# Kernel tuning notes

Measured on AMD Instinct MI355X. Metric: run time of the kernel, lower is better.

## Reference

```python
import jax, jax.numpy as jnp
import numpy as np

B, C_IN, C_OUT, K, H, W = 8, 512, 512, 3, 32, 32
EPS = 1e-8


def _fir_filter():
    f1 = jnp.array([1.0, 3.0, 3.0, 1.0], dtype=jnp.float32)
    f = jnp.outer(f1, f1)
    f = f / f.sum()
    return f * 4.0  # gain = 2**2, filter.ndim/2 == 1


def setup_inputs() -> dict:
    key = jax.random.key(0)
    k1, k2, k3 = jax.random.split(key, 3)
    x = jax.random.normal(k1, (B, C_IN, H, W), dtype=jnp.float32)
    styles = jax.random.normal(k2, (B, C_IN), dtype=jnp.float32)
    w = jax.random.normal(k3, (C_OUT, C_IN, K, K), dtype=jnp.float32)  # lr_multiplier=1
    return {"x": x, "styles": styles, "w": w}


def reference(x, styles, w):
    batch = x.shape[0]
    gain = 1.0 / np.sqrt(C_OUT * C_IN * K * K)
    # modulate: [B, O, I, kh, kw]
    wm = (w[None] * gain) * (styles[:, None, :, None, None] + 1.0)
    # demodulate
    dcoefs = jax.lax.rsqrt(jnp.sum(wm * wm, axis=(2, 3, 4)) + EPS)  # [B, O]
    wm = wm * dcoefs[:, :, None, None, None]
    # fused modconv: batch folded into channels/groups
    x1 = x.reshape(1, batch * C_IN, H, W)
    # torch conv_transpose2d(stride=2, padding=0, groups=B) == dilated conv with
    # spatially flipped kernel, lhs_dilation=2, padding=K-1 on each side.
    w_eq = jnp.flip(wm, axis=(-2, -1)).reshape(batch * C_OUT, C_IN, K, K)
    y = jax.lax.conv_general_dilated(
        x1, w_eq,
        window_strides=(1, 1),
        padding=[(K - 1, K - 1), (K - 1, K - 1)],
        lhs_dilation=(2, 2),
        feature_group_count=batch,
        dimension_numbers=("NCHW", "OIHW", "NCHW"),
    )  # [1, B*O, 2H+1, 2W+1]
    # Upfirdn2d: up=1, down=1, pad=[1,1,1,1], depthwise 4x4 FIR (cross-correlation;
    # filter is symmetric so no flip needed)
    C = batch * C_OUT
    f = jnp.broadcast_to(_fir_filter()[None, None], (C, 1, 4, 4))
    y = jax.lax.conv_general_dilated(
        y, f,
        window_strides=(1, 1),
        padding=[(1, 1), (1, 1)],
        feature_group_count=C,
        dimension_numbers=("NCHW", "OIHW", "NCHW"),
    )  # [1, B*O, 2H, 2W]
    return y.reshape(batch, C_OUT, 2 * H, 2 * W)
```

## Files before the change

### kernel.cpp

```cpp
#include <hip/hip_runtime.h>
#include <stdint.h>


#define DI __device__ __forceinline__

typedef __bf16 bf16x8 __attribute__((ext_vector_type(8)));
typedef float f32x4 __attribute__((ext_vector_type(4)));

DI float bf2f(ushort u) { union { uint32_t i; float f; } v; v.i = ((uint32_t)u) << 16; return v.f; }
DI ushort f2bf(float f) {
  union { float f; uint32_t i; } v; v.f = f;
  uint32_t x = v.i;
  return (ushort)((x + 0x7FFFu + ((x >> 16) & 1u)) >> 16);
}

#define GAIN (1.0f / 1536.0f)

__global__ __launch_bounds__(256) void k_prep(const float* __restrict__ w,
                                              const float* __restrict__ styles,
                                              const float* __restrict__ x,
                                              ushort* __restrict__ Wm,
                                              ushort* __restrict__ xt) {
  __shared__ union {
    struct { float ss[4096]; float dc[8]; float wred[4][8]; } wp;
    float tl[32][257];
  } sm;
  const int t = threadIdx.x;
  if (blockIdx.x < 512) {
    const int o = blockIdx.x;
#pragma unroll
    for (int j = 0; j < 4; j++) {
      const int idx = (t + j * 256) * 4;
      *(float4*)&sm.wp.ss[idx] = *(const float4*)&styles[idx];
    }
    float wreg[18];
    const float* wp_ = w + o * 4608 + t * 18;
#pragma unroll
    for (int k = 0; k < 9; k++) {
      float2 v2 = *(const float2*)(wp_ + 2 * k);
      wreg[2 * k] = v2.x;
      wreg[2 * k + 1] = v2.y;
    }
    float q0 = 0.f, q1 = 0.f;
#pragma unroll
    for (int k = 0; k < 9; k++) {
      q0 += wreg[k] * wreg[k];
      q1 += wreg[9 + k] * wreg[9 + k];
    }
    __syncthreads();
    float pb[8];
#pragma unroll
    for (int b = 0; b < 8; b++) {
      float s0 = sm.wp.ss[b * 512 + 2 * t] + 1.0f;
      float s1 = sm.wp.ss[b * 512 + 2 * t + 1] + 1.0f;
      pb[b] = s0 * s0 * q0 + s1 * s1 * q1;
    }
#pragma unroll
    for (int b = 0; b < 8; b++)
#pragma unroll
      for (int off = 32; off > 0; off >>= 1) pb[b] += __shfl_down(pb[b], off, 64);
    const int wid = t >> 6, lane = t & 63;
    if (lane == 0) {
#pragma unroll
      for (int b = 0; b < 8; b++) sm.wp.wred[wid][b] = pb[b];
    }
    __syncthreads();
    if (t < 8)
      sm.wp.dc[t] = rsqrtf((sm.wp.wred[0][t] + sm.wp.wred[1][t] + sm.wp.wred[2][t] + sm.wp.wred[3][t]) *
                               (GAIN * GAIN) + 1e-8f);
    __syncthreads();
#pragma unroll
    for (int b = 0; b < 8; b++) {
      const float d = sm.wp.dc[b];
      const float s0 = GAIN * (sm.wp.ss[b * 512 + 2 * t] + 1.0f) * d;
      const float s1 = GAIN * (sm.wp.ss[b * 512 + 2 * t + 1] + 1.0f) * d;
      ushort* base = Wm + ((size_t)(b * 9) * 512 + o) * 512 + 2 * t;
#pragma unroll
      for (int tap = 0; tap < 9; tap++) {
        ushort2 val = make_ushort2(f2bf(wreg[tap] * s0), f2bf(wreg[9 + tap] * s1));
        *(ushort2*)(base + (size_t)tap * 262144) = val;
      }
    }
  } else {
    const int idx = blockIdx.x - 512;
    const int hw0 = (idx & 3) * 256, i0 = ((idx >> 2) & 15) * 32, b = idx >> 6;
    const float* xb = x + b * (512 * 1024);
#pragma unroll
    for (int p = 0; p < 8; p++) {
      const int r = p * 4 + (t >> 6);
      const int c4 = (t & 63) * 4;
      float4 v = *(const float4*)&xb[(i0 + r) * 1024 + hw0 + c4];
      sm.tl[r][c4] = v.x; sm.tl[r][c4 + 1] = v.y; sm.tl[r][c4 + 2] = v.z; sm.tl[r][c4 + 3] = v.w;
    }
    __syncthreads();
    ushort* xtb = xt + b * (1024 * 512);
#pragma unroll
    for (int p = 0; p < 8; p++) {
      const int hw = p * 32 + (t >> 3);
      const int i4 = (t & 7) * 4;
      ushort4 v = make_ushort4(f2bf(sm.tl[i4][hw]), f2bf(sm.tl[i4 + 1][hw]),
                               f2bf(sm.tl[i4 + 2][hw]), f2bf(sm.tl[i4 + 3][hw]));
      *(ushort4*)&xtb[(hw0 + hw) * 512 + i0 + i4] = v;
    }
  }
}

__global__ __launch_bounds__(512, 4) void k_gemm(const ushort* __restrict__ A,
                                                 const ushort* __restrict__ Bt,
                                                 ushort* __restrict__ C) {
  __shared__ __attribute__((aligned(128))) char smem[49152];
  const int id = blockIdx.x;
  const int batch = id & 7;
  const int rem = id >> 3;
  const int mt = rem >> 2, nt = rem & 3;
  const int m0 = mt * 128, n0 = nt * 256;
  const ushort* Ag = A + (size_t)batch * (4608 * 512);
  const ushort* Bg = Bt + (size_t)batch * (1024 * 512);
  ushort* Cg = C + (size_t)batch * (4608 * 1024);

  const int tid = threadIdx.x;
  const int w = tid >> 6, lane = tid & 63;
  const int wm = w >> 2, wn = w & 3;
  const int lq = lane >> 4, l15 = lane & 15;

  const int srow = lane >> 2;
  const int sslot = (lane & 3) ^ ((lane >> 3) & 3);
  const char* gsrc[3];
  int ldst[3];
#pragma unroll
  for (int q = 0; q < 3; ++q) {
    const int idx = 3 * w + q;
    const bool isA = idx < 8;
    const int ch = isA ? idx : idx - 8;
    const int grow = (isA ? m0 : n0) + ch * 16 + srow;
    gsrc[q] = (const char*)(isA ? Ag : Bg) + (size_t)grow * 1024 + sslot * 16;
    ldst[q] = (isA ? 0 : 8192) + ch * 1024;
  }

#define GLL(srcp, dstp)                                                                     \
  __builtin_amdgcn_global_load_lds((const __attribute__((address_space(1))) void*)(srcp),   \
                                   (__attribute__((address_space(3))) void*)(dstp), 16, 0, 0)
#define ISSUE(buf, kt)                                              \
  do {                                                              \
    _Pragma("unroll")                                               \
    for (int q = 0; q < 3; ++q)                                     \
      GLL(gsrc[q] + (kt) * 64, smem + (buf) * 24576 + ldst[q]);     \
  } while (0)
#define CF asm volatile("" ::: "memory")
#define BAR()                          \
  do {                                 \
    CF;                                \
    __builtin_amdgcn_s_barrier();      \
    CF;                                \
  } while (0)

  const int so = (lq ^ ((l15 >> 1) & 3)) * 16;
  const char* Ard = smem + (wm * 64 + l15) * 64 + so;
  const char* Brd = smem + 8192 + (wn * 64 + l15) * 64 + so;

  f32x4 acc[4][4];
  const f32x4 z4 = {0.f, 0.f, 0.f, 0.f};
#pragma unroll
  for (int i = 0; i < 4; ++i)
#pragma unroll
    for (int n = 0; n < 4; ++n) acc[i][n] = z4;

  ISSUE(0, 0);
  asm volatile("s_waitcnt vmcnt(0)" ::: "memory");
  BAR();

#pragma unroll 2
  for (int t = 0; t < 16; ++t) {
    const int buf = t & 1;
    if (t < 15) ISSUE(buf ^ 1, t + 1);
    bf16x8 a[4], b[4];
#pragma unroll
    for (int i = 0; i < 4; ++i) a[i] = *(const bf16x8*)(Ard + buf * 24576 + i * 1024);
#pragma unroll
    for (int n = 0; n < 4; ++n) b[n] = *(const bf16x8*)(Brd + buf * 24576 + n * 1024);
    __builtin_amdgcn_s_setprio(1);
#pragma unroll
    for (int n = 0; n < 4; ++n)
#pragma unroll
      for (int i = 0; i < 4; ++i)
        acc[i][n] = __builtin_amdgcn_mfma_f32_16x16x32_bf16(a[i], b[n], acc[i][n], 0, 0, 0);
    __builtin_amdgcn_s_setprio(0);
    if (t < 15) asm volatile("s_waitcnt vmcnt(0)" ::: "memory");
    BAR();
  }

  ushort* cs = (ushort*)smem;
#pragma unroll
  for (int p = 0; p < 2; ++p) {
    if (p) BAR();
    if (wm == p) {
#pragma unroll
      for (int mi = 0; mi < 4; ++mi)
#pragma unroll
        for (int n = 0; n < 4; ++n) {
          const int row = mi * 16 + lq * 4;
          const int col = wn * 64 + n * 16 + l15;
          const f32x4 v = acc[mi][n];
#pragma unroll
          for (int r = 0; r < 4; ++r) cs[(row + r) * 264 + col] = f2bf(v[r]);
        }
    }
    BAR();
#pragma unroll
    for (int j = 0; j < 4; ++j) {
      const int idx = j * 512 + tid;
      const int row = idx >> 5, c = idx & 31;
      *(uint4*)(Cg + (size_t)(m0 + p * 64 + row) * 1024 + n0 + c * 8) =
          *(const uint4*)(cs + row * 264 + c * 8);
    }
  }
#undef GLL
#undef ISSUE
#undef CF
#undef BAR
}

__global__ __launch_bounds__(512) void k_fir(const ushort* __restrict__ C,
                                             float* __restrict__ out) {
  const int bo = blockIdx.x;
  const int b = bo >> 9, o = bo & 511;
  __shared__ __attribute__((aligned(16))) ushort Ct[9 * 1024];
  __shared__ float V[3 * 64 * 36];
  const ushort* Cb = C + ((size_t)(b * 9) * 512 + o) * 1024;
  for (int c = threadIdx.x; c < 1152; c += 512) {
    const int tap = c >> 7, off = (c & 127) * 8;
    *(uint4*)&Ct[tap * 1024 + off] = *(const uint4*)&Cb[(size_t)tap * 524288 + off];
  }
  __syncthreads();
#pragma unroll
  for (int j = 0; j < 3; j++) {
    const int gidx = threadIdx.x + j * 512;
    const int kw = gidx >> 9;
    const int rem = gidx & 511;
    const int u = rem >> 3;
    const int w0 = (rem & 7) * 4;
    float a0 = 0.f, a1 = 0.f, a2 = 0.f, a3 = 0.f;
#pragma unroll
    for (int kh = 0; kh < 3; kh++) {
      const int s0 = (kh + 1 + u) & 1;
#pragma unroll
      for (int d = 0; d < 2; d++) {
        const int h = (u + s0 + 2 * d - 1 - kh) >> 1;
        const bool ok = (h >= 0) & (h < 32);
        const float cf = ok ? ((s0 == d) ? 1.f : 3.f) : 0.f;
        const int hh = ok ? h : 0;
        const uint2 cv = *(const uint2*)&Ct[kh * 3072 + kw * 1024 + hh * 32 + w0];
        a0 += cf * bf2f((ushort)(cv.x & 0xffff));
        a1 += cf * bf2f((ushort)(cv.x >> 16));
        a2 += cf * bf2f((ushort)(cv.y & 0xffff));
        a3 += cf * bf2f((ushort)(cv.y >> 16));
      }
    }
    *(float4*)&V[kw * 2304 + u * 36 + w0] = make_float4(a0, a1, a2, a3);
  }
  __syncthreads();
  const size_t ob = (size_t)bo * 4096;
#pragma unroll
  for (int j = 0; j < 2; j++) {
    const int px4 = threadIdx.x + j * 512;
    const int u = px4 >> 4;
    const int v0 = (px4 & 15) * 4;
    float r[4] = {0.f, 0.f, 0.f, 0.f};
#pragma unroll
    for (int q = 0; q < 4; q++) {
      const int v = v0 + q;
#pragma unroll
      for (int kw = 0; kw < 3; kw++) {
        const int t0 = (kw + 1 + v) & 1;
#pragma unroll
        for (int d = 0; d < 2; d++) {
          const int wx = (v + t0 + 2 * d - 1 - kw) >> 1;
          const bool ok = (wx >= 0) & (wx < 32);
          const float cf = ok ? ((t0 == d) ? 1.f : 3.f) : 0.f;
          const int ww = ok ? wx : 0;
          r[q] += cf * V[kw * 2304 + u * 36 + ww];
        }
      }
      r[q] *= 0.0625f;
    }
    *(float4*)&out[ob + u * 64 + v0] = make_float4(r[0], r[1], r[2], r[3]);
  }
}

extern "C" void kernel_launch(void* const* d_in, const int* in_sizes, int n_in,
                              void* d_out, int out_size, void* d_ws, size_t ws_size,
                              hipStream_t stream) {
  (void)in_sizes; (void)n_in; (void)out_size; (void)ws_size;
  const float* x = (const float*)d_in[0];
  const float* styles = (const float*)d_in[1];
  const float* w = (const float*)d_in[2];
  float* out = (float*)d_out;
  char* ws = (char*)d_ws;
  ushort* Wm = (ushort*)ws;
  ushort* XT = (ushort*)(ws + 37748736);
  ushort* C = (ushort*)(ws + 37748736 + 8388608);

  k_prep<<<1024, 256, 0, stream>>>(w, styles, x, Wm, XT);
  k_gemm<<<1152, 512, 0, stream>>>(Wm, XT, C);
  k_fir<<<4096, 512, 0, stream>>>(C, out);
}
```

Before: 163.5 us.

## Split GEMM k-step into two phases with staggered async LDS loads

Restructures the bf16 MFMA GEMM main loop so each k-step runs in two halves (B columns 0-1, then 2-3). Global-to-LDS loads for the next tiles are issued between the halves, and A/B01 tiles are prefetched two steps ahead with partial vmcnt waits instead of draining all loads each iteration. The LDS swizzle pattern changes to match the new per-warp chunk assignment. Each iteration now has more barriers, and the lookahead logic is more intricate, which could hurt if the barriers serialize the warps.

Measured after the change: 160.2 us. 2.0% less time.

```diff
diff --git a/kernel.cpp b/kernel.cpp
--- a/kernel.cpp
+++ b/kernel.cpp
@@ -124,28 +124,19 @@
   const int lq = lane >> 4, l15 = lane & 15;
 
   const int srow = lane >> 2;
-  const int sslot = (lane & 3) ^ ((lane >> 3) & 3);
-  const char* gsrc[3];
-  int ldst[3];
-#pragma unroll
-  for (int q = 0; q < 3; ++q) {
-    const int idx = 3 * w + q;
-    const bool isA = idx < 8;
-    const int ch = isA ? idx : idx - 8;
-    const int grow = (isA ? m0 : n0) + ch * 16 + srow;
-    gsrc[q] = (const char*)(isA ? Ag : Bg) + (size_t)grow * 1024 + sslot * 16;
-    ldst[q] = (isA ? 0 : 8192) + ch * 1024;
-  }
+  const int ssw = (lane & 3) ^ ((lane >> 2) & 3);
+  const int cb01 = (w >> 1) * 4 + (w & 1);
+  const int cb23 = cb01 + 2;
+  const char* pa = (const char*)Ag + (size_t)(m0 + w * 16 + srow) * 1024 + ssw * 16;
+  const char* pb01 = (const char*)Bg + (size_t)(n0 + cb01 * 16 + srow) * 1024 + ssw * 16;
+  const char* pb23 = (const char*)Bg + (size_t)(n0 + cb23 * 16 + srow) * 1024 + ssw * 16;
+  char* da = smem + w * 1024;
+  char* db01 = smem + 8192 + cb01 * 1024;
+  char* db23 = smem + 8192 + cb23 * 1024;
 
 #define GLL(srcp, dstp)                                                                     \
   __builtin_amdgcn_global_load_lds((const __attribute__((address_space(1))) void*)(srcp),   \
                                    (__attribute__((address_space(3))) void*)(dstp), 16, 0, 0)
-#define ISSUE(buf, kt)                                              \
-  do {                                                              \
-    _Pragma("unroll")                                               \
-    for (int q = 0; q < 3; ++q)                                     \
-      GLL(gsrc[q] + (kt) * 64, smem + (buf) * 24576 + ldst[q]);     \
-  } while (0)
 #define CF asm volatile("" ::: "memory")
 #define BAR()                          \
   do {                                 \
@@ -154,7 +145,7 @@
     CF;                                \
   } while (0)
 
-  const int so = (lq ^ ((l15 >> 1) & 3)) * 16;
+  const int so = (lq ^ (l15 & 3)) * 16;
   const char* Ard = smem + (wm * 64 + l15) * 64 + so;
   const char* Brd = smem + 8192 + (wn * 64 + l15) * 64 + so;
 
@@ -165,27 +156,50 @@
 #pragma unroll
     for (int n = 0; n < 4; ++n) acc[i][n] = z4;
 
-  ISSUE(0, 0);
-  asm volatile("s_waitcnt vmcnt(0)" ::: "memory");
+  GLL(pa, da); GLL(pb01, db01); GLL(pb23, db23);
+  GLL(pa + 64, da + 24576); GLL(pb01 + 64, db01 + 24576);
+  asm volatile("s_waitcnt vmcnt(2)" ::: "memory");
   BAR();
 
-#pragma unroll 2
+#pragma unroll
   for (int t = 0; t < 16; ++t) {
     const int buf = t & 1;
-    if (t < 15) ISSUE(buf ^ 1, t + 1);
-    bf16x8 a[4], b[4];
-#pragma unroll
-    for (int i = 0; i < 4; ++i) a[i] = *(const bf16x8*)(Ard + buf * 24576 + i * 1024);
-#pragma unroll
-    for (int n = 0; n < 4; ++n) b[n] = *(const bf16x8*)(Brd + buf * 24576 + n * 1024);
+    const char* Ab = Ard + buf * 24576;
+    const char* Bb = Brd + buf * 24576;
+    bf16x8 a[4], bv[2], bw[2];
+#pragma unroll
+    for (int i = 0; i < 4; ++i) a[i] = *(const bf16x8*)(Ab + i * 1024);
+    bv[0] = *(const bf16x8*)(Bb);
+    bv[1] = *(const bf16x8*)(Bb + 1024);
+    if (t < 15) GLL(pb23 + (t + 1) * 64, db23 + (buf ^ 1) * 24576);
+    BAR();
     __builtin_amdgcn_s_setprio(1);
 #pragma unroll
-    for (int n = 0; n < 4; ++n)
+    for (int n = 0; n < 2; ++n)
 #pragma unroll
       for (int i = 0; i < 4; ++i)
-        acc[i][n] = __builtin_amdgcn_mfma_f32_16x16x32_bf16(a[i], b[n], acc[i][n], 0, 0, 0);
+        acc[i][n] = __builtin_amdgcn_mfma_f32_16x16x32_bf16(a[i], bv[n], acc[i][n], 0, 0, 0);
     __builtin_amdgcn_s_setprio(0);
-    if (t < 15) asm volatile("s_waitcnt vmcnt(0)" ::: "memory");
+    BAR();
+    bw[0] = *(const bf16x8*)(Bb + 2048);
+    bw[1] = *(const bf16x8*)(Bb + 3072);
+    if (t < 14) {
+      GLL(pa + (t + 2) * 64, da + buf * 24576);
+      GLL(pb01 + (t + 2) * 64, db01 + buf * 24576);
+    }
+    BAR();
+    __builtin_amdgcn_s_setprio(1);
+#pragma unroll
+    for (int n = 0; n < 2; ++n)
+#pragma unroll
+      for (int i = 0; i < 4; ++i)
+        acc[i][2 + n] = __builtin_amdgcn_mfma_f32_16x16x32_bf16(a[i], bw[n], acc[i][2 + n], 0, 0, 0);
+    __builtin_amdgcn_s_setprio(0);
+    if (t < 14) {
+      asm volatile("s_waitcnt vmcnt(2)" ::: "memory");
+    } else if (t == 14) {
+      asm volatile("s_waitcnt vmcnt(0)" ::: "memory");
+    }
     BAR();
   }
 
@@ -215,7 +229,6 @@
     }
   }
 #undef GLL
-#undef ISSUE
 #undef CF
 #undef BAR
 }
```
